# Kernel optimization log

Measured on AMD Instinct MI355X. Metric: run time of the kernel, lower is better.

## Reference

```python
import jax, jax.numpy as jnp
import numpy as np

B, IN_CH, OUT_CH, N_GRID, MODES = 64, 64, 64, 2048, 512


def _dct1_matrix(N, dtype=jnp.float32):
    """Matrix M s.t. (x @ M.T) == scipy.fftpack.dct(x, type=1, axis=-1).
    DCT-I: y[k] = x[0] + (-1)^k x[N-1] + 2*sum_{n=1}^{N-2} x[n] cos(pi k n/(N-1)).
    Note scipy's unnormalized idct(type=1) is the same transform, so M also
    implements chebyshev_inverse."""
    k = jnp.arange(N, dtype=jnp.float32)
    M = jnp.cos(jnp.pi * jnp.outer(k, k) / (N - 1))
    c = jnp.full((N,), 2.0, dtype=jnp.float32).at[0].set(1.0).at[N - 1].set(1.0)
    return (M * c[None, :]).astype(dtype)


def setup_inputs() -> dict:
    key = jax.random.key(0)
    kx, kw = jax.random.split(key)
    x = jax.random.normal(kx, (B, IN_CH, N_GRID), dtype=jnp.float32)
    # xavier_uniform on (in, out, modes): fan_in=in, fan_out=out (per torch for 3D params)
    bound = float(np.sqrt(6.0 / (IN_CH + OUT_CH)))
    weights = jax.random.uniform(kw, (IN_CH, OUT_CH, MODES), minval=-bound,
                                 maxval=bound, dtype=jnp.float32)
    return {"x": x, "weights": weights}


def reference(x, weights):
    # x: [b, in, n]; weights: [in, out, modes]
    N = x.shape[-1]
    modes = weights.shape[-1]
    M = _dct1_matrix(N, x.dtype)
    # forward Chebyshev (DCT-I) transform along grid axis
    x_cheb = jnp.einsum('bin,kn->bik', x, M)          # [b, in, n]
    # mix modes: keep first `modes` coefficients, zero the rest
    out_modes = jnp.einsum('bix,iox->box', x_cheb[..., :modes], weights)
    out_cheb = jnp.pad(out_modes, ((0, 0), (0, 0), (0, N - modes)))
    # inverse transform (scipy unnormalized IDCT-I == DCT-I)
    return jnp.einsum('bok,nk->bon', out_cheb, M)     # [b, out, n]
```

## Files before the change

### kernel.cpp

```cpp
#include <hip/hip_runtime.h>

typedef unsigned short u16;
typedef __attribute__((ext_vector_type(8))) short short8;
typedef __attribute__((ext_vector_type(4))) float f32x4;

#define B_  64
#define IC  64
#define OC  64
#define NG  2048
#define MD  512

__device__ inline u16 f2b(float f) {
  unsigned u = __float_as_uint(f);
  unsigned r = (u + 0x7FFFu + ((u >> 16) & 1u)) >> 16;
  return (u16)r;
}

__device__ __forceinline__ void gld_lds16(const u16* g, const u16* l) {
  __builtin_amdgcn_global_load_lds(
      (__attribute__((address_space(1))) void*)(uintptr_t)(g),
      (__attribute__((address_space(3))) void*)(unsigned)(uintptr_t)(l),
      16, 0, 0);
}

__global__ __launch_bounds__(256) void cast_bf16(const float* __restrict__ in,
                                                 u16* __restrict__ out) {
  int i = (blockIdx.x * 256 + threadIdx.x) * 4;
  float4 v = *(const float4*)(in + i);
  ushort4 o;
  o.x = f2b(v.x); o.y = f2b(v.y); o.z = f2b(v.z); o.w = f2b(v.w);
  *(ushort4*)(out + i) = o;
}

__global__ __launch_bounds__(256) void build_M1(u16* __restrict__ M1) {
  int idx = blockIdx.x * 256 + threadIdx.x;
  int k = idx >> 11, n = idx & 2047;
  int r = (k * n) % (2 * (NG - 1));
  float ang = (float)r * (3.14159265358979323846f / (NG - 1));
  float v = __cosf(ang) * ((n == 0 || n == NG - 1) ? 1.0f : 2.0f);
  M1[idx] = f2b(v);
}

__global__ __launch_bounds__(256) void build_M3(u16* __restrict__ M3) {
  int idx = blockIdx.x * 256 + threadIdx.x;
  int n = idx >> 9, k = idx & 511;
  int r = (n * k) % (2 * (NG - 1));
  float ang = (float)r * (3.14159265358979323846f / (NG - 1));
  float v = __cosf(ang) * ((k == 0) ? 1.0f : 2.0f);
  M3[idx] = f2b(v);
}

template<int MI, int NI>
__global__ __launch_bounds__(256, 2) void gemm_bt2(
    const u16* __restrict__ A,
    const u16* __restrict__ Bt,
    float* __restrict__ C,
    int K, int N) {
  constexpr int TM = MI * 32;
  constexpr int TN = NI * 32;
  constexpr int BK = 64;
  constexpr int ROWS = TM + TN;
  constexpr int CH = ROWS / 4;
  constexpr int NISSUE = CH / 8;
  __shared__ u16 S[ROWS * BK];

  const int tid  = threadIdx.x;
  const int lane = tid & 63;
  const int wave = tid >> 6;
  const int wm = (wave >> 1) * (MI * 16);
  const int wn = (wave & 1) * (NI * 16);
  const long bm = (long)blockIdx.y * TM;
  const long bn = (long)blockIdx.x * TN;

  const int lrow = lane & 15;
  const int lhi  = lane >> 4;

  const int scc = (((lane & 7) ^ (lane >> 3)) * 8);
  const int r0 = wave * CH;

  const u16* gsrc[NISSUE];
  const u16* ldst[NISSUE];
#pragma unroll
  for (int ii = 0; ii < NISSUE; ++ii) {
    int rr = r0 + ii * 8 + (lane >> 3);
    gsrc[ii] = (rr < TM) ? (A + (bm + rr) * (long)K + scc)
                         : (Bt + (bn + rr - TM) * (long)K + scc);
    ldst[ii] = &S[(r0 + ii * 8) * BK];
  }

  f32x4 acc[MI][NI] = {};

  for (int k0 = 0; k0 < K; k0 += BK) {
#pragma unroll
    for (int ii = 0; ii < NISSUE; ++ii)
      gld_lds16(gsrc[ii] + k0, ldst[ii]);
    __syncthreads();

#pragma unroll
    for (int kk8 = 0; kk8 < 8; kk8 += 4) {
      short8 af[MI], bfr[NI];
#pragma unroll
      for (int i = 0; i < MI; ++i) {
        int pch = ((kk8 + lhi) ^ (lane & 7));
        af[i] = *(const short8*)&S[(wm + i * 16 + lrow) * BK + pch * 8];
      }
#pragma unroll
      for (int j = 0; j < NI; ++j) {
        int pch = ((kk8 + lhi) ^ (lane & 7));
        bfr[j] = *(const short8*)&S[(TM + wn + j * 16 + lrow) * BK + pch * 8];
      }
#pragma unroll
      for (int i = 0; i < MI; ++i)
#pragma unroll
        for (int j = 0; j < NI; ++j)
          acc[i][j] = __builtin_amdgcn_mfma_f32_16x16x32_bf16(af[i], bfr[j], acc[i][j], 0, 0, 0);
    }
    __syncthreads();
  }

  const int crow = (lane >> 4) * 4;
  const int ccol = lane & 15;
#pragma unroll
  for (int i = 0; i < MI; ++i)
#pragma unroll
    for (int j = 0; j < NI; ++j) {
      long gm = bm + wm + i * 16 + crow;
      long gn = bn + wn + j * 16 + ccol;
      float* cp = C + gm * (long)N + gn;
#pragma unroll
      for (int r = 0; r < 4; ++r)
        cp[(long)r * N] = acc[i][j][r];
    }
}

__global__ __launch_bounds__(256) void transpose_w(const float* __restrict__ w,
                                                   float* __restrict__ wT) {
  __shared__ float S[64][65];
  const int ib = blockIdx.x;
  const int kb = blockIdx.y;
  const int t = threadIdx.x;
  const int r0 = t >> 6;
  const int c  = t & 63;
#pragma unroll
  for (int j = 0; j < 16; ++j) {
    int r = r0 + j * 4;
    S[r][c] = w[(size_t)(ib * 64 + r) * MD + kb * 64 + c];
  }
  __syncthreads();
#pragma unroll
  for (int j = 0; j < 16; ++j) {
    int r = r0 + j * 4;
    wT[(size_t)(kb * 64 + r) * 4096 + ib * 64 + c] = S[c][r];
  }
}

__global__ __launch_bounds__(256, 4) void mode_mix(
    const float* __restrict__ xcT,
    const float* __restrict__ wT,
    u16* __restrict__ omT) {
  __shared__ float Lxc[4096];
  __shared__ float Lw[4096];
  const int k = blockIdx.x;
  const int t = threadIdx.x;
#pragma unroll
  for (int j = 0; j < 16; ++j) {
    int idx = t + j * 256;
    Lxc[idx] = xcT[(size_t)k * 4096 + idx];
    Lw[idx]  = wT[(size_t)k * 4096 + idx];
  }
  __syncthreads();

  const int b0 = (t >> 4) << 2;
  const int o0 = (t & 15) << 2;
  float acc[4][4] = {};
  for (int i = 0; i < 64; ++i) {
    float xv0 = Lxc[(b0 + 0) * 64 + i];
    float xv1 = Lxc[(b0 + 1) * 64 + i];
    float xv2 = Lxc[(b0 + 2) * 64 + i];
    float xv3 = Lxc[(b0 + 3) * 64 + i];
    float4 wv = *(const float4*)&Lw[i * 64 + o0];
    acc[0][0] += xv0 * wv.x; acc[0][1] += xv0 * wv.y; acc[0][2] += xv0 * wv.z; acc[0][3] += xv0 * wv.w;
    acc[1][0] += xv1 * wv.x; acc[1][1] += xv1 * wv.y; acc[1][2] += xv1 * wv.z; acc[1][3] += xv1 * wv.w;
    acc[2][0] += xv2 * wv.x; acc[2][1] += xv2 * wv.y; acc[2][2] += xv2 * wv.z; acc[2][3] += xv2 * wv.w;
    acc[3][0] += xv3 * wv.x; acc[3][1] += xv3 * wv.y; acc[3][2] += xv3 * wv.z; acc[3][3] += xv3 * wv.w;
  }
#pragma unroll
  for (int r = 0; r < 4; ++r) {
    ushort4 p;
    p.x = f2b(acc[r][0]); p.y = f2b(acc[r][1]); p.z = f2b(acc[r][2]); p.w = f2b(acc[r][3]);
    *(ushort4*)&omT[(size_t)k * 4096 + (b0 + r) * 64 + o0] = p;
  }
}

__global__ __launch_bounds__(256) void transpose_om(const u16* __restrict__ omT,
                                                    u16* __restrict__ om) {
  __shared__ u16 S[64][65];
  const int bb = blockIdx.x;
  const int kb = blockIdx.y;
  const int t = threadIdx.x;
  const int r0 = t >> 6;
  const int c  = t & 63;
#pragma unroll
  for (int j = 0; j < 16; ++j) {
    int kr = r0 + j * 4;
    S[kr][c] = omT[(size_t)(kb * 64 + kr) * 4096 + bb * 64 + c];
  }
  __syncthreads();
#pragma unroll
  for (int j = 0; j < 16; ++j) {
    int br = r0 + j * 4;
    om[(size_t)(bb * 64 + br) * MD + kb * 64 + c] = S[c][br];
  }
}

extern "C" void kernel_launch(void* const* d_in, const int* in_sizes, int n_in,
                              void* d_out, int out_size, void* d_ws, size_t ws_size,
                              hipStream_t stream) {
  const float* x = (const float*)d_in[0];
  const float* w = (const float*)d_in[1];
  float* out = (float*)d_out;

  char* ws = (char*)d_ws;
  u16*   xb  = (u16*)ws;
  float* wT  = (float*)ws;
  u16*   omT = (u16*)(ws + (size_t)8 * 1024 * 1024);
  u16*   om  = (u16*)(ws + (size_t)12 * 1024 * 1024);
  u16*   M1  = (u16*)(ws + (size_t)16 * 1024 * 1024);
  u16*   M3  = (u16*)(ws + (size_t)18 * 1024 * 1024);
  float* xcT = (float*)(ws + (size_t)20 * 1024 * 1024);

  cast_bf16<<<(B_ * IC * NG / 4) / 256, 256, 0, stream>>>(x, xb);
  build_M1<<<(MD * NG) / 256, 256, 0, stream>>>(M1);
  build_M3<<<(NG * MD) / 256, 256, 0, stream>>>(M3);

  gemm_bt2<2, 2><<<dim3((B_ * IC) / 64, MD / 64), 256, 0, stream>>>(M1, xb, xcT, NG, B_ * IC);

  transpose_w<<<dim3(64, 8), 256, 0, stream>>>(w, wT);

  mode_mix<<<MD, 256, 0, stream>>>(xcT, wT, omT);

  transpose_om<<<dim3((B_ * OC) / 64, MD / 64), 256, 0, stream>>>(omT, om);

  gemm_bt2<4, 4><<<dim3(NG / 128, (B_ * OC) / 128), 256, 0, stream>>>(om, M3, out, MD, NG);
}
```

Measured before the change: 146.5 us.

## Fuse prep kernels, store xcT in bf16, and run mode mixing on MFMA

Merges the input cast, weight transpose and both DCT matrix builds into one prep launch, with the weights transposed into bf16 and laid out [k][o][i]. The forward GEMM now writes its output in bf16, halving that intermediate's traffic. The per-mode 64x64x64 mixing uses bf16 MFMA instead of scalar FP32 FMAs. This removes launches and memory traffic but adds rounding of the intermediate coefficients and the weights to bf16, which costs accuracy.

New measurement: 133.1 us. 9.2% less time.

```diff
diff --git a/kernel.cpp b/kernel.cpp
--- a/kernel.cpp
+++ b/kernel.cpp
@@ -23,38 +23,56 @@
       16, 0, 0);
 }
 
-__global__ __launch_bounds__(256) void cast_bf16(const float* __restrict__ in,
-                                                 u16* __restrict__ out) {
-  int i = (blockIdx.x * 256 + threadIdx.x) * 4;
-  float4 v = *(const float4*)(in + i);
-  ushort4 o;
-  o.x = f2b(v.x); o.y = f2b(v.y); o.z = f2b(v.z); o.w = f2b(v.w);
-  *(ushort4*)(out + i) = o;
-}
-
-__global__ __launch_bounds__(256) void build_M1(u16* __restrict__ M1) {
-  int idx = blockIdx.x * 256 + threadIdx.x;
-  int k = idx >> 11, n = idx & 2047;
-  int r = (k * n) % (2 * (NG - 1));
-  float ang = (float)r * (3.14159265358979323846f / (NG - 1));
-  float v = __cosf(ang) * ((n == 0 || n == NG - 1) ? 1.0f : 2.0f);
-  M1[idx] = f2b(v);
-}
-
-__global__ __launch_bounds__(256) void build_M3(u16* __restrict__ M3) {
-  int idx = blockIdx.x * 256 + threadIdx.x;
-  int n = idx >> 9, k = idx & 511;
-  int r = (n * k) % (2 * (NG - 1));
-  float ang = (float)r * (3.14159265358979323846f / (NG - 1));
-  float v = __cosf(ang) * ((k == 0) ? 1.0f : 2.0f);
-  M3[idx] = f2b(v);
-}
-
-template<int MI, int NI>
+__global__ __launch_bounds__(256) void prep(
+    const float* __restrict__ x, const float* __restrict__ w,
+    u16* __restrict__ xb, u16* __restrict__ wT2,
+    u16* __restrict__ M1, u16* __restrict__ M3) {
+  __shared__ float S[64][65];
+  const int id = blockIdx.x;
+  const int t = threadIdx.x;
+  if (id < 8192) {
+    int i = (id * 256 + t) * 4;
+    float4 v = *(const float4*)(x + i);
+    ushort4 o;
+    o.x = f2b(v.x); o.y = f2b(v.y); o.z = f2b(v.z); o.w = f2b(v.w);
+    *(ushort4*)(xb + i) = o;
+  } else if (id < 8704) {
+    int wb = id - 8192;
+    int o = wb & 63, kb = wb >> 6;
+    int r0 = t >> 6, c = t & 63;
+#pragma unroll
+    for (int j = 0; j < 16; ++j) {
+      int i = r0 + j * 4;
+      S[i][c] = w[(size_t)(i * 64 + o) * MD + kb * 64 + c];
+    }
+    __syncthreads();
+#pragma unroll
+    for (int j = 0; j < 16; ++j) {
+      int kk = r0 + j * 4;
+      wT2[(size_t)(kb * 64 + kk) * 4096 + o * 64 + c] = f2b(S[c][kk]);
+    }
+  } else if (id < 12800) {
+    int idx = (id - 8704) * 256 + t;
+    int k = idx >> 11, n = idx & 2047;
+    int r = (k * n) % (2 * (NG - 1));
+    float ang = (float)r * (3.14159265358979323846f / (NG - 1));
+    float v = __cosf(ang) * ((n == 0 || n == NG - 1) ? 1.0f : 2.0f);
+    M1[idx] = f2b(v);
+  } else {
+    int idx = (id - 12800) * 256 + t;
+    int n = idx >> 9, k = idx & 511;
+    int r = (n * k) % (2 * (NG - 1));
+    float ang = (float)r * (3.14159265358979323846f / (NG - 1));
+    float v = __cosf(ang) * ((k == 0) ? 1.0f : 2.0f);
+    M3[idx] = f2b(v);
+  }
+}
+
+template<int MI, int NI, bool OUT_BF16>
 __global__ __launch_bounds__(256, 2) void gemm_bt2(
     const u16* __restrict__ A,
     const u16* __restrict__ Bt,
-    float* __restrict__ C,
+    void* __restrict__ Cv,
     int K, int N) {
   constexpr int TM = MI * 32;
   constexpr int TN = NI * 32;
@@ -126,70 +144,76 @@
     for (int j = 0; j < NI; ++j) {
       long gm = bm + wm + i * 16 + crow;
       long gn = bn + wn + j * 16 + ccol;
-      float* cp = C + gm * (long)N + gn;
-#pragma unroll
-      for (int r = 0; r < 4; ++r)
-        cp[(long)r * N] = acc[i][j][r];
-    }
-}
-
-__global__ __launch_bounds__(256) void transpose_w(const float* __restrict__ w,
-                                                   float* __restrict__ wT) {
-  __shared__ float S[64][65];
-  const int ib = blockIdx.x;
-  const int kb = blockIdx.y;
-  const int t = threadIdx.x;
-  const int r0 = t >> 6;
-  const int c  = t & 63;
-#pragma unroll
-  for (int j = 0; j < 16; ++j) {
-    int r = r0 + j * 4;
-    S[r][c] = w[(size_t)(ib * 64 + r) * MD + kb * 64 + c];
-  }
-  __syncthreads();
-#pragma unroll
-  for (int j = 0; j < 16; ++j) {
-    int r = r0 + j * 4;
-    wT[(size_t)(kb * 64 + r) * 4096 + ib * 64 + c] = S[c][r];
-  }
-}
-
-__global__ __launch_bounds__(256, 4) void mode_mix(
-    const float* __restrict__ xcT,
-    const float* __restrict__ wT,
+      if (OUT_BF16) {
+        u16* cp = (u16*)Cv + gm * (long)N + gn;
+#pragma unroll
+        for (int r = 0; r < 4; ++r)
+          cp[(long)r * N] = f2b(acc[i][j][r]);
+      } else {
+        float* cp = (float*)Cv + gm * (long)N + gn;
+#pragma unroll
+        for (int r = 0; r < 4; ++r)
+          cp[(long)r * N] = acc[i][j][r];
+      }
+    }
+}
+
+__global__ __launch_bounds__(256, 4) void mode_mix_mfma(
+    const u16* __restrict__ xcT,
+    const u16* __restrict__ wT2,
     u16* __restrict__ omT) {
-  __shared__ float Lxc[4096];
-  __shared__ float Lw[4096];
+  constexpr int PK = 72;
+  __shared__ u16 S[128 * PK];
   const int k = blockIdx.x;
   const int t = threadIdx.x;
-#pragma unroll
-  for (int j = 0; j < 16; ++j) {
-    int idx = t + j * 256;
-    Lxc[idx] = xcT[(size_t)k * 4096 + idx];
-    Lw[idx]  = wT[(size_t)k * 4096 + idx];
+
+#pragma unroll
+  for (int c = 0; c < 4; ++c) {
+    int ch = t + c * 256;
+    int half = ch >> 9, cc = ch & 511;
+    int row = cc >> 3, col8 = cc & 7;
+    const u16* src = half ? wT2 : xcT;
+    uint4 v = *(const uint4*)(src + (size_t)k * 4096 + row * 64 + col8 * 8);
+    *(uint4*)&S[(half * 64 + row) * PK + col8 * 8] = v;
   }
   __syncthreads();
 
-  const int b0 = (t >> 4) << 2;
-  const int o0 = (t & 15) << 2;
-  float acc[4][4] = {};
-  for (int i = 0; i < 64; ++i) {
-    float xv0 = Lxc[(b0 + 0) * 64 + i];
-    float xv1 = Lxc[(b0 + 1) * 64 + i];
-    float xv2 = Lxc[(b0 + 2) * 64 + i];
-    float xv3 = Lxc[(b0 + 3) * 64 + i];
-    float4 wv = *(const float4*)&Lw[i * 64 + o0];
-    acc[0][0] += xv0 * wv.x; acc[0][1] += xv0 * wv.y; acc[0][2] += xv0 * wv.z; acc[0][3] += xv0 * wv.w;
-    acc[1][0] += xv1 * wv.x; acc[1][1] += xv1 * wv.y; acc[1][2] += xv1 * wv.z; acc[1][3] += xv1 * wv.w;
-    acc[2][0] += xv2 * wv.x; acc[2][1] += xv2 * wv.y; acc[2][2] += xv2 * wv.z; acc[2][3] += xv2 * wv.w;
-    acc[3][0] += xv3 * wv.x; acc[3][1] += xv3 * wv.y; acc[3][2] += xv3 * wv.z; acc[3][3] += xv3 * wv.w;
-  }
-#pragma unroll
-  for (int r = 0; r < 4; ++r) {
-    ushort4 p;
-    p.x = f2b(acc[r][0]); p.y = f2b(acc[r][1]); p.z = f2b(acc[r][2]); p.w = f2b(acc[r][3]);
-    *(ushort4*)&omT[(size_t)k * 4096 + (b0 + r) * 64 + o0] = p;
-  }
+  const int lane = t & 63;
+  const int wave = t >> 6;
+  const int wm = (wave >> 1) * 32;
+  const int wn = (wave & 1) * 32;
+  const int lrow = lane & 15;
+  const int lhi  = lane >> 4;
+
+  f32x4 acc[2][2] = {};
+#pragma unroll
+  for (int kk8 = 0; kk8 < 8; kk8 += 4) {
+    short8 af[2], bfr[2];
+#pragma unroll
+    for (int i = 0; i < 2; ++i)
+      af[i] = *(const short8*)&S[(wm + i * 16 + lrow) * PK + (kk8 + lhi) * 8];
+#pragma unroll
+    for (int j = 0; j < 2; ++j)
+      bfr[j] = *(const short8*)&S[(64 + wn + j * 16 + lrow) * PK + (kk8 + lhi) * 8];
+#pragma unroll
+    for (int i = 0; i < 2; ++i)
+#pragma unroll
+      for (int j = 0; j < 2; ++j)
+        acc[i][j] = __builtin_amdgcn_mfma_f32_16x16x32_bf16(af[i], bfr[j], acc[i][j], 0, 0, 0);
+  }
+
+  const int crow = (lane >> 4) * 4;
+  const int ccol = lane & 15;
+#pragma unroll
+  for (int i = 0; i < 2; ++i)
+#pragma unroll
+    for (int j = 0; j < 2; ++j) {
+      int b = wm + i * 16 + crow;
+      int o = wn + j * 16 + ccol;
+#pragma unroll
+      for (int r = 0; r < 4; ++r)
+        omT[(size_t)k * 4096 + (b + r) * 64 + o] = f2b(acc[i][j][r]);
+    }
 }
 
 __global__ __launch_bounds__(256) void transpose_om(const u16* __restrict__ omT,
@@ -221,25 +245,23 @@
   float* out = (float*)d_out;
 
   char* ws = (char*)d_ws;
-  u16*   xb  = (u16*)ws;
-  float* wT  = (float*)ws;
-  u16*   omT = (u16*)(ws + (size_t)8 * 1024 * 1024);
-  u16*   om  = (u16*)(ws + (size_t)12 * 1024 * 1024);
-  u16*   M1  = (u16*)(ws + (size_t)16 * 1024 * 1024);
-  u16*   M3  = (u16*)(ws + (size_t)18 * 1024 * 1024);
-  float* xcT = (float*)(ws + (size_t)20 * 1024 * 1024);
-
-  cast_bf16<<<(B_ * IC * NG / 4) / 256, 256, 0, stream>>>(x, xb);
-  build_M1<<<(MD * NG) / 256, 256, 0, stream>>>(M1);
-  build_M3<<<(NG * MD) / 256, 256, 0, stream>>>(M3);
-
-  gemm_bt2<2, 2><<<dim3((B_ * IC) / 64, MD / 64), 256, 0, stream>>>(M1, xb, xcT, NG, B_ * IC);
-
-  transpose_w<<<dim3(64, 8), 256, 0, stream>>>(w, wT);
-
-  mode_mix<<<MD, 256, 0, stream>>>(xcT, wT, omT);
+  u16* xb  = (u16*)ws;
+  u16* M1  = (u16*)(ws + (size_t)16 * 1024 * 1024);
+  u16* M3  = (u16*)(ws + (size_t)18 * 1024 * 1024);
+  u16* xcT = (u16*)(ws + (size_t)20 * 1024 * 1024);
+  u16* wT2 = (u16*)(ws + (size_t)24 * 1024 * 1024);
+  u16* omT = (u16*)(ws + (size_t)28 * 1024 * 1024);
+  u16* om  = (u16*)(ws + (size_t)32 * 1024 * 1024);
+
+  prep<<<16896, 256, 0, stream>>>(x, w, xb, wT2, M1, M3);
+
+  gemm_bt2<2, 2, true><<<dim3((B_ * IC) / 64, MD / 64), 256, 0, stream>>>(
+      M1, xb, xcT, NG, B_ * IC);
+
+  mode_mix_mfma<<<MD, 256, 0, stream>>>(xcT, wT2, omT);
 
   transpose_om<<<dim3((B_ * OC) / 64, MD / 64), 256, 0, stream>>>(omT, om);
 
-  gemm_bt2<4, 4><<<dim3(NG / 128, (B_ * OC) / 128), 256, 0, stream>>>(om, M3, out, MD, NG);
-}
+  gemm_bt2<4, 4, false><<<dim3(NG / 128, (B_ * OC) / 128), 256, 0, stream>>>(
+      om, M3, out, MD, NG);
+}
```
